# Optimization experiments

Measured on AMD Instinct MI355X. Metric: run time of the kernel, lower is better.

Reference implementation:

```python
import jax, jax.numpy as jnp
import numpy as np

NUM_NODES = 50000
NUM_EDGES = 400000
NUM_GRAPHS = 16


def _glorot(key, shape):
    fan_in, fan_out = shape[0], shape[1]
    lim = jnp.sqrt(6.0 / (fan_in + fan_out))
    return jax.random.uniform(key, shape, jnp.float32, -lim, lim)


def setup_inputs() -> dict:
    key = jax.random.key(0)
    ks = jax.random.split(key, 12)
    x = jax.random.normal(ks[0], (NUM_NODES, 3), jnp.float32)
    edge_index = jax.random.randint(ks[1], (2, NUM_EDGES), 0, NUM_NODES, jnp.int64)
    batch = jax.random.randint(ks[2], (NUM_NODES,), 0, NUM_GRAPHS, jnp.int64)
    return {
        "x": x,
        "edge_index": edge_index,
        "batch": batch,
        "W1": _glorot(ks[3], (3, 512)),   "b1": jnp.zeros((512,), jnp.float32),
        "W2": _glorot(ks[4], (512, 1024)), "b2": jnp.zeros((1024,), jnp.float32),
        "W3": _glorot(ks[5], (1024, 512)), "b3": jnp.zeros((512,), jnp.float32),
        "fcw1": _glorot(ks[6], (512, 128)), "fcb1": jnp.zeros((128,), jnp.float32),
        "fcw2": _glorot(ks[7], (128, 1)),   "fcb2": jnp.zeros((1,), jnp.float32),
    }


def _gcn_conv(x, W, b, row, col, n):
    # PyG GCNConv: h = x W; out_i = sum_{j->i} d_j^{-1/2} d_i^{-1/2} h_j + b
    # (row, col) already include self-loops; edge weights are 1.
    h = x @ W  # [N, out]
    deg = jnp.zeros((n,), h.dtype).at[col].add(1.0)  # in-degree incl. self-loop
    dis = jax.lax.rsqrt(deg)  # deg >= 1 thanks to self-loops
    norm = dis[row] * dis[col]  # [E]
    msgs = h[row] * norm[:, None]  # [E, out] gather
    return jax.ops.segment_sum(msgs, col, num_segments=n) + b


def reference(x, edge_index, batch, W1, b1, W2, b2, W3, b3, fcw1, fcb1, fcw2, fcb2):
    n = x.shape[0]
    loop = jnp.arange(n, dtype=edge_index.dtype)
    row = jnp.concatenate([edge_index[0], loop])  # source
    col = jnp.concatenate([edge_index[1], loop])  # target

    h = jax.nn.relu(_gcn_conv(x, W1, b1, row, col, n))
    h = jax.nn.relu(_gcn_conv(h, W2, b2, row, col, n))
    h = jax.nn.relu(_gcn_conv(h, W3, b3, row, col, n))

    # global mean pool over graphs in the batch
    sums = jax.ops.segment_sum(h, batch, num_segments=NUM_GRAPHS)  # [G, 512]
    cnts = jax.ops.segment_sum(jnp.ones((n,), h.dtype), batch, num_segments=NUM_GRAPHS)
    pooled = sums / jnp.maximum(cnts, 1.0)[:, None]

    out = jax.nn.relu(pooled @ fcw1 + fcb1)
    out = out @ fcw2 + fcb2  # [G, 1]
    return out
```

## Files before the change

### kernel.cpp

```cpp
#include <hip/hip_runtime.h>
#include <hip/hip_bf16.h>

#define NNODES 50000
#define NEDGES 400000
#define NGRAPH 16

typedef __attribute__((ext_vector_type(4))) float floatx4;
typedef __attribute__((ext_vector_type(8))) short short8;

typedef __attribute__((address_space(3))) unsigned int lds_uint;
typedef __attribute__((address_space(1))) const unsigned int gbl_uint;

__device__ __forceinline__ void load16_to_lds(const void* g, void* l) {
    __builtin_amdgcn_global_load_lds((gbl_uint*)g, (lds_uint*)l, 16, 0, 0);
}

__global__ __launch_bounds__(64) void zero_out_k(float* out, int n) {
    int i = blockIdx.x * 64 + threadIdx.x;
    if (i < n) out[i] = 0.0f;
}

__global__ __launch_bounds__(256) void init_k(int* deg_cnt, int* cursor,
                                              float* gsum, int* gcnt,
                                              const float* __restrict__ x,
                                              float4* __restrict__ xp, int n) {
    int i = blockIdx.x * 256 + threadIdx.x;
    if (i < n) {
        deg_cnt[i] = 0; cursor[i] = 0;
        xp[i] = make_float4(x[i * 3 + 0], x[i * 3 + 1], x[i * 3 + 2], 0.0f);
    }
    if (i < NGRAPH * 512) gsum[i] = 0.0f;
    if (i < NGRAPH) gcnt[i] = 0;
}

__global__ __launch_bounds__(256) void deg_k(const int* __restrict__ col,
                                             int* __restrict__ deg_cnt, int e) {
    int i = blockIdx.x * 256 + threadIdx.x;
    if (i < e) atomicAdd(&deg_cnt[col[i]], 1);
}

__global__ __launch_bounds__(256) void segsum_k(const int* __restrict__ cnt,
                                                int* __restrict__ segsum, int n) {
    __shared__ int sb[256];
    int seg = blockIdx.x;
    int base = seg * 1024;
    int t = threadIdx.x;
    int s = 0;
#pragma unroll
    for (int j = 0; j < 4; ++j) {
        int idx = base + t + j * 256;
        if (idx < n) s += cnt[idx];
    }
    sb[t] = s;
    __syncthreads();
    for (int off = 128; off > 0; off >>= 1) {
        if (t < off) sb[t] += sb[t + off];
        __syncthreads();
    }
    if (t == 0) segsum[seg] = sb[0];
}

__global__ __launch_bounds__(64) void segscan_k(const int* __restrict__ segsum,
                                                int* __restrict__ segbase,
                                                int* __restrict__ offs,
                                                int nseg, int n) {
    if (threadIdx.x == 0) {
        int run = 0;
        for (int s = 0; s < nseg; ++s) { segbase[s] = run; run += segsum[s]; }
        offs[n] = run;
    }
}

__global__ __launch_bounds__(1024) void offs_k(const int* __restrict__ cnt,
                                               const int* __restrict__ segbase,
                                               int* __restrict__ offs,
                                               float* __restrict__ dis, int n) {
    __shared__ int sb[1024];
    int seg = blockIdx.x;
    int t = threadIdx.x;
    int i = seg * 1024 + t;
    int c = (i < n) ? cnt[i] : 0;
    sb[t] = c;
    __syncthreads();
    for (int off = 1; off < 1024; off <<= 1) {
        int v = (t >= off) ? sb[t - off] : 0;
        __syncthreads();
        sb[t] += v;
        __syncthreads();
    }
    if (i < n) {
        offs[i] = segbase[seg] + sb[t] - c;
        dis[i]  = rsqrtf((float)(c + 1));
    }
}

__global__ __launch_bounds__(256) void scatter_k(const int* __restrict__ row,
                                                 const int* __restrict__ col,
                                                 const int* __restrict__ offs,
                                                 int* __restrict__ cursor,
                                                 int* __restrict__ ssrc,
                                                 float* __restrict__ sw,
                                                 const float* __restrict__ dis, int e) {
    int i = blockIdx.x * 256 + threadIdx.x;
    if (i >= e) return;
    int d = col[i];
    int p = offs[d] + atomicAdd(&cursor[d], 1);
    int s = row[i];
    ssrc[p] = s;
    sw[p]   = dis[s];
}

__global__ __launch_bounds__(256) void agg3_k(const float4* __restrict__ xp,
                                              float* __restrict__ out,
                                              const int* __restrict__ offs,
                                              const int* __restrict__ ssrc,
                                              const float* __restrict__ sw,
                                              const float* __restrict__ dis, int n) {
    int d = blockIdx.x * 256 + threadIdx.x;
    if (d >= n) return;
    float dd = dis[d];
    float4 xd = xp[d];
    float a0 = dd * xd.x, a1 = dd * xd.y, a2 = dd * xd.z;
    int beg = offs[d], end = offs[d + 1];
    for (int e = beg; e < end; ++e) {
        int s = ssrc[e];
        float w = sw[e];
        float4 q = xp[s];
        a0 += w * q.x; a1 += w * q.y; a2 += w * q.z;
    }
    out[d * 3 + 0] = dd * a0;
    out[d * 3 + 1] = dd * a1;
    out[d * 3 + 2] = dd * a2;
}

__global__ __launch_bounds__(256) void gemm1_k(const float* __restrict__ aggx,
                                               const float* __restrict__ W1,
                                               const float* __restrict__ b1,
                                               __hip_bfloat16* __restrict__ h1, int n) {
    int wave = threadIdx.x >> 6;
    int lane = threadIdx.x & 63;
    int d = blockIdx.x * 4 + wave;
    if (d >= n) return;
    float a0 = aggx[d * 3 + 0], a1 = aggx[d * 3 + 1], a2 = aggx[d * 3 + 2];
    int f0 = lane * 8;
    short8 ov;
#pragma unroll
    for (int j = 0; j < 8; ++j) {
        int f = f0 + j;
        float v = b1[f] + a0 * W1[f] + a1 * W1[512 + f] + a2 * W1[1024 + f];
        __hip_bfloat16 h = __float2bfloat16(fmaxf(v, 0.0f));
        ov[j] = *(short*)&h;
    }
    *(short8*)&h1[(size_t)d * 512 + f0] = ov;
}

__device__ inline float bs2f(short v) {
    return __uint_as_float(((unsigned int)(unsigned short)v) << 16);
}

__global__ __launch_bounds__(256) void agg512w_k(const __hip_bfloat16* __restrict__ in,
                                                 __hip_bfloat16* __restrict__ out,
                                                 const int* __restrict__ offs,
                                                 const int* __restrict__ ssrc,
                                                 const float* __restrict__ sw,
                                                 const float* __restrict__ dis,
                                                 const float* __restrict__ bias,
                                                 int relu, int n) {
    int wave = threadIdx.x >> 6;
    int lane = threadIdx.x & 63;
    int d = blockIdx.x * 4 + wave;
    if (d >= n) return;
    float dd = dis[d];
    short8 p = *(const short8*)&in[(size_t)d * 512 + lane * 8];
    float acc[8];
#pragma unroll
    for (int j = 0; j < 8; ++j) acc[j] = dd * bs2f(p[j]);

    int beg = offs[d], end = offs[d + 1];
    int e = beg;
    for (; e + 3 < end; e += 4) {
        int s0 = ssrc[e],     s1 = ssrc[e + 1];
        int s2 = ssrc[e + 2], s3 = ssrc[e + 3];
        float w0 = sw[e],     w1 = sw[e + 1];
        float w2 = sw[e + 2], w3 = sw[e + 3];
        short8 q0 = *(const short8*)&in[(size_t)s0 * 512 + lane * 8];
        short8 q1 = *(const short8*)&in[(size_t)s1 * 512 + lane * 8];
        short8 q2 = *(const short8*)&in[(size_t)s2 * 512 + lane * 8];
        short8 q3 = *(const short8*)&in[(size_t)s3 * 512 + lane * 8];
#pragma unroll
        for (int j = 0; j < 8; ++j) acc[j] += w0 * bs2f(q0[j]);
#pragma unroll
        for (int j = 0; j < 8; ++j) acc[j] += w1 * bs2f(q1[j]);
#pragma unroll
        for (int j = 0; j < 8; ++j) acc[j] += w2 * bs2f(q2[j]);
#pragma unroll
        for (int j = 0; j < 8; ++j) acc[j] += w3 * bs2f(q3[j]);
    }
    for (; e < end; ++e) {
        int s0 = ssrc[e];
        float w0 = sw[e];
        short8 q0 = *(const short8*)&in[(size_t)s0 * 512 + lane * 8];
#pragma unroll
        for (int j = 0; j < 8; ++j) acc[j] += w0 * bs2f(q0[j]);
    }

    short8 ov;
#pragma unroll
    for (int j = 0; j < 8; ++j) {
        float v = acc[j] * dd;
        if (bias) v += bias[lane * 8 + j];
        if (relu) v = fmaxf(v, 0.0f);
        __hip_bfloat16 h = __float2bfloat16(v);
        ov[j] = *(short*)&h;
    }
    *(short8*)&out[(size_t)d * 512 + lane * 8] = ov;
}

__global__ __launch_bounds__(256) void tcvt_k(const float* __restrict__ W2,
                                              __hip_bfloat16* __restrict__ w2t,
                                              const float* __restrict__ W3,
                                              __hip_bfloat16* __restrict__ w3t) {
    __shared__ float tile[32][33];
    int t = threadIdx.x;
    const float* W; __hip_bfloat16* Wt;
    int K, N, idx;
    if (blockIdx.x < 512) { W = W2; Wt = w2t; K = 512;  N = 1024; idx = blockIdx.x; }
    else                  { W = W3; Wt = w3t; K = 1024; N = 512;  idx = blockIdx.x - 512; }
    int nbn = N / 32;
    int bn = (idx % nbn) * 32;
    int bk = (idx / nbn) * 32;
    int c = t & 31, r0 = t >> 5;
#pragma unroll
    for (int j = 0; j < 4; ++j) {
        int r = r0 + j * 8;
        tile[r][c] = W[(size_t)(bk + r) * N + bn + c];
    }
    __syncthreads();
#pragma unroll
    for (int j = 0; j < 4; ++j) {
        int r = r0 + j * 8;
        Wt[(size_t)(bn + r) * K + bk + c] = __float2bfloat16(tile[c][r]);
    }
}

__global__ __launch_bounds__(512, 2) void mfma_gemm256_k(
        const __hip_bfloat16* __restrict__ A,
        const __hip_bfloat16* __restrict__ Bt,
        const float* __restrict__ bias,
        __hip_bfloat16* __restrict__ C,
        int M, int N, int K, int relu, int lnt) {
    __shared__ short smem[65536];

    int tid  = threadIdx.x;
    int lane = tid & 63;
    int wave = tid >> 6;
    int wm = wave >> 2;
    int wn = wave & 3;
    int fr = lane & 15;
    int kg = lane >> 4;
    int f7 = fr & 7;

    int nwg = gridDim.x;
    int wg  = (blockIdx.x & 7) * (nwg >> 3) + (blockIdx.x >> 3);
    int mt  = wg >> lnt;
    int nt  = wg & ((1 << lnt) - 1);
    int bm  = mt << 8;
    int bn  = nt << 8;

    int rsub = lane >> 3;
    int slog = (lane & 7) ^ rsub;
    const __hip_bfloat16* ga[4];
    const __hip_bfloat16* gb[4];
#pragma unroll
    for (int j = 0; j < 4; ++j) {
        int rloc = (wave * 4 + j) * 8 + rsub;
        ga[j] = A  + (size_t)(bm + rloc) * K + slog * 8;
        gb[j] = Bt + (size_t)(bn + rloc) * K + slog * 8;
    }
    int dstA = wave * 2048;

    int aoff = (wm * 128 + fr) * 64 + ((kg ^ f7) * 8);
    int boff = 16384 + (wn * 64 + fr) * 64 + ((kg ^ f7) * 8);

    floatx4 acc[8][4] = {};

    auto stage = [&](int p) {
        short* sp = &smem[p * 32768];
#pragma unroll
        for (int j = 0; j < 4; ++j) {
            load16_to_lds(ga[j], sp + dstA + j * 512);
            load16_to_lds(gb[j], sp + 16384 + dstA + j * 512);
            ga[j] += 64;
            gb[j] += 64;
        }
    };

    stage(0);
    int KT = K >> 6;
    for (int t = 0; t < KT; ++t) {
        int p = t & 1;
        __builtin_amdgcn_s_barrier();
        if (t + 1 < KT) {
            stage(p ^ 1);
            asm volatile("s_waitcnt vmcnt(8)" ::: "memory");
        } else {
            asm volatile("s_waitcnt vmcnt(0)" ::: "memory");
        }
        __builtin_amdgcn_s_barrier();

        const short* sm = &smem[p * 32768];
#pragma unroll
        for (int ks = 0; ks < 2; ++ks) {
            int kx = ks * 32;
            short8 bfr[4];
#pragma unroll
            for (int ni = 0; ni < 4; ++ni)
                bfr[ni] = *(const short8*)&sm[(boff + ni * 1024) ^ kx];
#pragma unroll
            for (int mh = 0; mh < 2; ++mh) {
                short8 afr[4];
#pragma unroll
                for (int mi = 0; mi < 4; ++mi)
                    afr[mi] = *(const short8*)&sm[(aoff + (mh * 4 + mi) * 1024) ^ kx];
                __builtin_amdgcn_s_setprio(1);
#pragma unroll
                for (int mi = 0; mi < 4; ++mi)
#pragma unroll
                    for (int ni = 0; ni < 4; ++ni)
                        acc[mh * 4 + mi][ni] = __builtin_amdgcn_mfma_f32_16x16x32_bf16(
                            afr[mi], bfr[ni], acc[mh * 4 + mi][ni], 0, 0, 0);
                __builtin_amdgcn_s_setprio(0);
            }
        }
    }

    short* Cs = smem;
    int l4 = lane >> 4;
#pragma unroll
    for (int h = 0; h < 2; ++h) {
        __builtin_amdgcn_s_barrier();
        if (wm == h) {
#pragma unroll
            for (int mi = 0; mi < 8; ++mi) {
#pragma unroll
                for (int ni = 0; ni < 4; ++ni) {
                    int rr = mi * 16 + l4 * 4;
                    int cc = wn * 64 + ni * 16 + fr;
                    float bv = bias ? bias[bn + cc] : 0.0f;
#pragma unroll
                    for (int r = 0; r < 4; ++r) {
                        float v = acc[mi][ni][r] + bv;
                        if (relu) v = fmaxf(v, 0.0f);
                        __hip_bfloat16 hh = __float2bfloat16(v);
                        Cs[(rr + r) * 264 + cc] = *(short*)&hh;
                    }
                }
            }
        }
        __builtin_amdgcn_s_barrier();
#pragma unroll
        for (int i = 0; i < 8; ++i) {
            int idx = tid + 512 * i;
            int rr = idx >> 5, cc = idx & 31;
            int grow = bm + h * 128 + rr;
            if (grow < M)
                *(short8*)&C[(size_t)grow * N + bn + cc * 8] =
                    *(const short8*)&Cs[rr * 264 + cc * 8];
        }
    }
}

__global__ __launch_bounds__(256) void pool_k(const __hip_bfloat16* __restrict__ h,
                                              const int* __restrict__ batch,
                                              float* __restrict__ gsum,
                                              int* __restrict__ gcnt, int n) {
    __shared__ float ls[NGRAPH * 512];
    __shared__ int lcnt[NGRAPH];
    int t = threadIdx.x;
    for (int i = t; i < NGRAPH * 512; i += 256) ls[i] = 0.0f;
    if (t < NGRAPH) lcnt[t] = 0;
    __syncthreads();
    for (int d = blockIdx.x; d < n; d += gridDim.x) {
        int g = batch[d];
        if (t == 0) atomicAdd(&lcnt[g], 1);
        unsigned int q = *(const unsigned int*)&h[(size_t)d * 512 + 2 * t];
        ls[g * 512 + 2 * t]     += __uint_as_float((q & 0xffffu) << 16);
        ls[g * 512 + 2 * t + 1] += __uint_as_float((q >> 16) << 16);
    }
    __syncthreads();
    for (int i = t; i < NGRAPH * 512; i += 256) atomicAdd(&gsum[i], ls[i]);
    if (t < NGRAPH) atomicAdd(&gcnt[t], lcnt[t]);
}

__global__ __launch_bounds__(128) void fc_k(const float* __restrict__ gsum,
                                            const int* __restrict__ gcnt,
                                            const float* __restrict__ fcw1,
                                            const float* __restrict__ fcb1,
                                            const float* __restrict__ fcw2,
                                            const float* __restrict__ fcb2,
                                            float* __restrict__ out) {
    int g = blockIdx.x;
    int t = threadIdx.x;
    __shared__ float pooled[512];
    __shared__ float red[128];
    float inv = 1.0f / fmaxf((float)gcnt[g], 1.0f);
    for (int i = t; i < 512; i += 128) pooled[i] = gsum[g * 512 + i] * inv;
    __syncthreads();
    float s = fcb1[t];
    for (int k = 0; k < 512; ++k) s += pooled[k] * fcw1[k * 128 + t];
    s = fmaxf(s, 0.0f);
    red[t] = s * fcw2[t];
    __syncthreads();
    for (int off = 64; off > 0; off >>= 1) {
        if (t < off) red[t] += red[t + off];
        __syncthreads();
    }
    if (t == 0) out[g] = red[0] + fcb2[0];
}

extern "C" void kernel_launch(void* const* d_in, const int* in_sizes, int n_in,
                              void* d_out, int out_size, void* d_ws, size_t ws_size,
                              hipStream_t stream) {
    const float* x    = (const float*)d_in[0];
    const int*   ei   = (const int*)d_in[1];
    const int*   batch= (const int*)d_in[2];
    const float* W1   = (const float*)d_in[3];
    const float* b1   = (const float*)d_in[4];
    const float* W2   = (const float*)d_in[5];
    const float* b2   = (const float*)d_in[6];
    const float* W3   = (const float*)d_in[7];
    const float* b3   = (const float*)d_in[8];
    const float* fcw1 = (const float*)d_in[9];
    const float* fcb1 = (const float*)d_in[10];
    const float* fcw2 = (const float*)d_in[11];
    const float* fcb2 = (const float*)d_in[12];
    float* out = (float*)d_out;

    const int N = in_sizes[0] / 3;
    const int E = in_sizes[1] / 2;
    const int Mpad = (N + 255) & ~255;
    const int nseg = (N + 1023) / 1024;
    const int* row = ei;
    const int* col = ei + E;

    size_t used = 0;
    auto need = [&](size_t bytes) {
        size_t off = used;
        used += (bytes + 255) & ~(size_t)255;
        return off;
    };
    size_t o_deg  = need((size_t)N * 4);
    size_t o_cur  = need((size_t)N * 4);
    size_t o_dis  = need((size_t)N * 4);
    size_t o_offs = need((size_t)(N + 1) * 4);
    size_t o_seg  = need((size_t)nseg * 4);
    size_t o_segb = need((size_t)nseg * 4);
    size_t o_ssrc = need((size_t)E * 4);
    size_t o_sw   = need((size_t)E * 4);
    size_t o_xp   = need((size_t)N * 16);
    size_t o_aggx = need((size_t)N * 3 * 4);
    size_t o_gsum = need((size_t)NGRAPH * 512 * 4);
    size_t o_gcnt = need((size_t)NGRAPH * 4);
    size_t o_w2t  = need((size_t)512 * 1024 * 2);
    size_t o_w3t  = need((size_t)1024 * 512 * 2);
    size_t o_bufX = need((size_t)Mpad * 512 * 2);
    size_t o_bufY = need((size_t)Mpad * 512 * 2);
    size_t o_bufZ = need((size_t)Mpad * 1024 * 2);

    if (used > ws_size) {
        hipLaunchKernelGGL(zero_out_k, dim3((out_size + 63) / 64), dim3(64), 0, stream,
                           out, out_size);
        return;
    }

    char* base = (char*)d_ws;
    int*    deg_cnt = (int*)   (base + o_deg);
    int*    cursor  = (int*)   (base + o_cur);
    float*  dis     = (float*) (base + o_dis);
    int*    offs    = (int*)   (base + o_offs);
    int*    segsum  = (int*)   (base + o_seg);
    int*    segbase = (int*)   (base + o_segb);
    int*    ssrc    = (int*)   (base + o_ssrc);
    float*  sw      = (float*) (base + o_sw);
    float4* xp      = (float4*)(base + o_xp);
    float*  aggx    = (float*) (base + o_aggx);
    float*  gsum    = (float*) (base + o_gsum);
    int*    gcnt    = (int*)   (base + o_gcnt);
    __hip_bfloat16* w2t  = (__hip_bfloat16*)(base + o_w2t);
    __hip_bfloat16* w3t  = (__hip_bfloat16*)(base + o_w3t);
    __hip_bfloat16* bufX = (__hip_bfloat16*)(base + o_bufX);
    __hip_bfloat16* bufY = (__hip_bfloat16*)(base + o_bufY);
    __hip_bfloat16* bufZ = (__hip_bfloat16*)(base + o_bufZ);
    (void)n_in;

    int gN = (N + 255) / 256;
    int gE = (E + 255) / 256;
    int gW = (N + 3) / 4;
    int nrt = Mpad / 256;

    hipLaunchKernelGGL(init_k, dim3(gN), dim3(256), 0, stream, deg_cnt, cursor, gsum, gcnt, x, xp, N);
    hipLaunchKernelGGL(deg_k, dim3(gE), dim3(256), 0, stream, col, deg_cnt, E);
    hipLaunchKernelGGL(segsum_k, dim3(nseg), dim3(256), 0, stream, deg_cnt, segsum, N);
    hipLaunchKernelGGL(segscan_k, dim3(1), dim3(64), 0, stream, segsum, segbase, offs, nseg, N);
    hipLaunchKernelGGL(offs_k, dim3(nseg), dim3(1024), 0, stream, deg_cnt, segbase, offs, dis, N);
    hipLaunchKernelGGL(scatter_k, dim3(gE), dim3(256), 0, stream, row, col, offs, cursor, ssrc, sw, dis, E);

    hipLaunchKernelGGL(tcvt_k, dim3(1024), dim3(256), 0, stream, W2, w2t, W3, w3t);

    hipLaunchKernelGGL(agg3_k, dim3(gN), dim3(256), 0, stream, xp, aggx, offs, ssrc, sw, dis, N);
    hipLaunchKernelGGL(gemm1_k, dim3(gW), dim3(256), 0, stream, aggx, W1, b1, bufX, N);

    hipLaunchKernelGGL(agg512w_k, dim3(gW), dim3(256), 0, stream, bufX, bufY, offs, ssrc, sw, dis,
                       (const float*)nullptr, 0, N);
    hipLaunchKernelGGL(mfma_gemm256_k, dim3(nrt * 4), dim3(512), 0, stream,
                       bufY, w2t, b2, bufZ, N, 1024, 512, 1, 2);

    hipLaunchKernelGGL(mfma_gemm256_k, dim3(nrt * 2), dim3(512), 0, stream,
                       bufZ, w3t, (const float*)nullptr, bufX, N, 512, 1024, 0, 1);
    hipLaunchKernelGGL(agg512w_k, dim3(gW), dim3(256), 0, stream, bufX, bufY, offs, ssrc, sw, dis,
                       b3, 1, N);

    hipLaunchKernelGGL(pool_k, dim3(256), dim3(256), 0, stream, bufY, batch, gsum, gcnt, N);
    hipLaunchKernelGGL(fc_k, dim3(NGRAPH), dim3(128), 0, stream, gsum, gcnt, fcw1, fcb1, fcw2, fcb2, out);
}
```

Baseline: 592.5 us.

## Switch GEMM to 4-stage K=32 pipeline with fragment-ordered LDS layout

The bf16 MFMA GEMM now stages K in chunks of 32 instead of 64 and keeps four LDS buffers in flight instead of two. Each global-to-LDS load writes a 16-row by 32-k subtile laid out so every lane can read its MFMA fragment contiguously, which removes the XOR swizzle. The intent is to hide global latency behind a deeper prefetch and simplify LDS addressing. The trade-off is twice as many barriers per K, and the unswizzled layout may cause LDS bank conflicts on the direct-to-LDS writes or the fragment reads.

```diff
diff --git a/kernel.cpp b/kernel.cpp
--- a/kernel.cpp
+++ b/kernel.cpp
@@ -257,8 +257,6 @@
     int wm = wave >> 2;
     int wn = wave & 3;
     int fr = lane & 15;
-    int kg = lane >> 4;
-    int f7 = fr & 7;
 
     int nwg = gridDim.x;
     int wg  = (blockIdx.x & 7) * (nwg >> 3) + (blockIdx.x >> 3);
@@ -267,72 +265,71 @@
     int bm  = mt << 8;
     int bn  = nt << 8;
 
-    int rsub = lane >> 3;
-    int slog = (lane & 7) ^ rsub;
-    const __hip_bfloat16* ga[4];
-    const __hip_bfloat16* gb[4];
-#pragma unroll
-    for (int j = 0; j < 4; ++j) {
-        int rloc = (wave * 4 + j) * 8 + rsub;
-        ga[j] = A  + (size_t)(bm + rloc) * K + slog * 8;
-        gb[j] = Bt + (size_t)(bn + rloc) * K + slog * 8;
-    }
-    int dstA = wave * 2048;
-
-    int aoff = (wm * 128 + fr) * 64 + ((kg ^ f7) * 8);
-    int boff = 16384 + (wn * 64 + fr) * 64 + ((kg ^ f7) * 8);
+    int r = lane & 15;
+    int s = lane >> 4;
+    const __hip_bfloat16* ga[2];
+    const __hip_bfloat16* gb[2];
+#pragma unroll
+    for (int j = 0; j < 2; ++j) {
+        int gsub = 2 * wave + j;
+        ga[j] = A  + (size_t)(bm + gsub * 16 + r) * K + s * 8;
+        gb[j] = Bt + (size_t)(bn + gsub * 16 + r) * K + s * 8;
+    }
 
     floatx4 acc[8][4] = {};
 
     auto stage = [&](int p) {
-        short* sp = &smem[p * 32768];
-#pragma unroll
-        for (int j = 0; j < 4; ++j) {
-            load16_to_lds(ga[j], sp + dstA + j * 512);
-            load16_to_lds(gb[j], sp + 16384 + dstA + j * 512);
-            ga[j] += 64;
-            gb[j] += 64;
+        short* sp = &smem[p * 16384];
+#pragma unroll
+        for (int j = 0; j < 2; ++j) {
+            load16_to_lds(ga[j], sp + (2 * wave + j) * 512);
+            load16_to_lds(gb[j], sp + 8192 + (2 * wave + j) * 512);
+            ga[j] += 32;
+            gb[j] += 32;
         }
     };
 
-    stage(0);
-    int KT = K >> 6;
-    for (int t = 0; t < KT; ++t) {
-        int p = t & 1;
+    auto compute = [&](int p) {
+        const short* sm = &smem[p * 16384];
+        short8 bfr[4];
+#pragma unroll
+        for (int ni = 0; ni < 4; ++ni)
+            bfr[ni] = *(const short8*)&sm[8192 + (wn * 4 + ni) * 512 + lane * 8];
+#pragma unroll
+        for (int mh = 0; mh < 2; ++mh) {
+            short8 afr[4];
+#pragma unroll
+            for (int mi = 0; mi < 4; ++mi)
+                afr[mi] = *(const short8*)&sm[(wm * 8 + mh * 4 + mi) * 512 + lane * 8];
+            __builtin_amdgcn_s_setprio(1);
+#pragma unroll
+            for (int mi = 0; mi < 4; ++mi)
+#pragma unroll
+                for (int ni = 0; ni < 4; ++ni)
+                    acc[mh * 4 + mi][ni] = __builtin_amdgcn_mfma_f32_16x16x32_bf16(
+                        afr[mi], bfr[ni], acc[mh * 4 + mi][ni], 0, 0, 0);
+            __builtin_amdgcn_s_setprio(0);
+        }
+    };
+
+    int KT = K >> 5;
+    stage(0); stage(1); stage(2);
+    for (int t = 0; t < KT - 3; ++t) {
+        stage((t + 3) & 3);
+        asm volatile("s_waitcnt vmcnt(12)" ::: "memory");
         __builtin_amdgcn_s_barrier();
-        if (t + 1 < KT) {
-            stage(p ^ 1);
-            asm volatile("s_waitcnt vmcnt(8)" ::: "memory");
-        } else {
-            asm volatile("s_waitcnt vmcnt(0)" ::: "memory");
-        }
+        compute(t & 3);
         __builtin_amdgcn_s_barrier();
-
-        const short* sm = &smem[p * 32768];
-#pragma unroll
-        for (int ks = 0; ks < 2; ++ks) {
-            int kx = ks * 32;
-            short8 bfr[4];
-#pragma unroll
-            for (int ni = 0; ni < 4; ++ni)
-                bfr[ni] = *(const short8*)&sm[(boff + ni * 1024) ^ kx];
-#pragma unroll
-            for (int mh = 0; mh < 2; ++mh) {
-                short8 afr[4];
-#pragma unroll
-                for (int mi = 0; mi < 4; ++mi)
-                    afr[mi] = *(const short8*)&sm[(aoff + (mh * 4 + mi) * 1024) ^ kx];
-                __builtin_amdgcn_s_setprio(1);
-#pragma unroll
-                for (int mi = 0; mi < 4; ++mi)
-#pragma unroll
-                    for (int ni = 0; ni < 4; ++ni)
-                        acc[mh * 4 + mi][ni] = __builtin_amdgcn_mfma_f32_16x16x32_bf16(
-                            afr[mi], bfr[ni], acc[mh * 4 + mi][ni], 0, 0, 0);
-                __builtin_amdgcn_s_setprio(0);
-            }
-        }
-    }
+    }
+    asm volatile("s_waitcnt vmcnt(8)" ::: "memory");
+    __builtin_amdgcn_s_barrier();
+    compute((KT - 3) & 3);
+    asm volatile("s_waitcnt vmcnt(4)" ::: "memory");
+    __builtin_amdgcn_s_barrier();
+    compute((KT - 2) & 3);
+    asm volatile("s_waitcnt vmcnt(0)" ::: "memory");
+    __builtin_amdgcn_s_barrier();
+    compute((KT - 1) & 3);
 
     short* Cs = smem;
     int l4 = lane >> 4;
@@ -348,11 +345,11 @@
                     int cc = wn * 64 + ni * 16 + fr;
                     float bv = bias ? bias[bn + cc] : 0.0f;
 #pragma unroll
-                    for (int r = 0; r < 4; ++r) {
-                        float v = acc[mi][ni][r] + bv;
+                    for (int q = 0; q < 4; ++q) {
+                        float v = acc[mi][ni][q] + bv;
                         if (relu) v = fmaxf(v, 0.0f);
                         __hip_bfloat16 hh = __float2bfloat16(v);
-                        Cs[(rr + r) * 264 + cc] = *(short*)&hh;
+                        Cs[(rr + q) * 264 + cc] = *(short*)&hh;
                     }
                 }
             }
@@ -406,10 +403,10 @@
     float inv = 1.0f / fmaxf((float)gcnt[g], 1.0f);
     for (int i = t; i < 512; i += 128) pooled[i] = gsum[g * 512 + i] * inv;
     __syncthreads();
-    float s = fcb1[t];
-    for (int k = 0; k < 512; ++k) s += pooled[k] * fcw1[k * 128 + t];
-    s = fmaxf(s, 0.0f);
-    red[t] = s * fcw2[t];
+    float sacc = fcb1[t];
+    for (int k = 0; k < 512; ++k) sacc += pooled[k] * fcw1[k * 128 + t];
+    sacc = fmaxf(sacc, 0.0f);
+    red[t] = sacc * fcw2[t];
     __syncthreads();
     for (int off = 64; off > 0; off >>= 1) {
         if (t < off) red[t] += red[t + off];
```

New measurement: 612.2 us. 3.3% more time.

## Fuse final GCN aggregation with global mean pooling via per-graph node permutation

Applied to the files above, without the earlier changes.

Builds a per-graph node permutation (count, prefix, place kernels) so the last aggregation can run grouped by graph. Bias, ReLU and pooling are applied in registers and reduced in LDS, then atomically added into the per-graph sums. This removes the write and re-read of the final 512-wide activation buffer and the separate pool kernel. It adds three small setup kernels and a memset, and the per-graph split may balance load unevenly across blocks. It also inserts an explicit LDS waitcnt before a barrier in the GEMM.

```diff
diff --git a/kernel.cpp b/kernel.cpp
--- a/kernel.cpp
+++ b/kernel.cpp
@@ -4,6 +4,7 @@
 #define NNODES 50000
 #define NEDGES 400000
 #define NGRAPH 16
+#define NBG 64
 
 typedef __attribute__((ext_vector_type(4))) float floatx4;
 typedef __attribute__((ext_vector_type(8))) short short8;
@@ -21,16 +22,23 @@
 }
 
 __global__ __launch_bounds__(256) void init_k(int* deg_cnt, int* cursor,
-                                              float* gsum, int* gcnt,
+                                              float* gsum, int* gdeg,
                                               const float* __restrict__ x,
-                                              float4* __restrict__ xp, int n) {
-    int i = blockIdx.x * 256 + threadIdx.x;
+                                              float4* __restrict__ xp,
+                                              const int* __restrict__ batch, int n) {
+    __shared__ int h[NGRAPH];
+    int t = threadIdx.x;
+    if (t < NGRAPH) h[t] = 0;
+    __syncthreads();
+    int i = blockIdx.x * 256 + t;
     if (i < n) {
         deg_cnt[i] = 0; cursor[i] = 0;
         xp[i] = make_float4(x[i * 3 + 0], x[i * 3 + 1], x[i * 3 + 2], 0.0f);
+        atomicAdd(&h[batch[i]], 1);
     }
     if (i < NGRAPH * 512) gsum[i] = 0.0f;
-    if (i < NGRAPH) gcnt[i] = 0;
+    __syncthreads();
+    if (t < NGRAPH && h[t]) atomicAdd(&gdeg[t], h[t]);
 }
 
 __global__ __launch_bounds__(256) void deg_k(const int* __restrict__ col,
@@ -108,6 +116,35 @@
     int s = row[i];
     ssrc[p] = s;
     sw[p]   = dis[s];
+}
+
+__global__ __launch_bounds__(64) void gpfx_k(const int* __restrict__ gdeg,
+                                             int* __restrict__ goffs) {
+    if (threadIdx.x == 0) {
+        int run = 0;
+        for (int g = 0; g < NGRAPH; ++g) { goffs[g] = run; run += gdeg[g]; }
+    }
+}
+
+__global__ __launch_bounds__(256) void gplace_k(const int* __restrict__ batch,
+                                                const int* __restrict__ goffs,
+                                                int* __restrict__ gcur,
+                                                int* __restrict__ perm, int n) {
+    __shared__ int h[NGRAPH];
+    __shared__ int basev[NGRAPH];
+    int t = threadIdx.x;
+    if (t < NGRAPH) h[t] = 0;
+    __syncthreads();
+    int i = blockIdx.x * 256 + t;
+    int g = 0, r = 0;
+    if (i < n) {
+        g = batch[i];
+        r = atomicAdd(&h[g], 1);
+    }
+    __syncthreads();
+    if (t < NGRAPH) basev[t] = h[t] ? atomicAdd(&gcur[t], h[t]) : 0;
+    __syncthreads();
+    if (i < n) perm[goffs[g] + basev[g] + r] = i;
 }
 
 __global__ __launch_bounds__(256) void agg3_k(const float4* __restrict__ xp,
@@ -163,9 +200,7 @@
                                                  const int* __restrict__ offs,
                                                  const int* __restrict__ ssrc,
                                                  const float* __restrict__ sw,
-                                                 const float* __restrict__ dis,
-                                                 const float* __restrict__ bias,
-                                                 int relu, int n) {
+                                                 const float* __restrict__ dis, int n) {
     int wave = threadIdx.x >> 6;
     int lane = threadIdx.x & 63;
     int d = blockIdx.x * 4 + wave;
@@ -207,13 +242,94 @@
     short8 ov;
 #pragma unroll
     for (int j = 0; j < 8; ++j) {
-        float v = acc[j] * dd;
-        if (bias) v += bias[lane * 8 + j];
-        if (relu) v = fmaxf(v, 0.0f);
-        __hip_bfloat16 h = __float2bfloat16(v);
+        __hip_bfloat16 h = __float2bfloat16(acc[j] * dd);
         ov[j] = *(short*)&h;
     }
     *(short8*)&out[(size_t)d * 512 + lane * 8] = ov;
+}
+
+__global__ __launch_bounds__(256) void aggpool_k(const __hip_bfloat16* __restrict__ in,
+                                                 const int* __restrict__ perm,
+                                                 const int* __restrict__ goffs,
+                                                 const int* __restrict__ gdeg,
+                                                 const int* __restrict__ offs,
+                                                 const int* __restrict__ ssrc,
+                                                 const float* __restrict__ sw,
+                                                 const float* __restrict__ dis,
+                                                 const float* __restrict__ bias,
+                                                 float* __restrict__ gsum) {
+    __shared__ float lsw[4 * 512];
+    int t = threadIdx.x;
+    int wave = t >> 6;
+    int lane = t & 63;
+    int g = blockIdx.x & (NGRAPH - 1);
+    int s = blockIdx.x >> 4;
+    for (int i = t; i < 4 * 512; i += 256) lsw[i] = 0.0f;
+    int cnt = gdeg[g];
+    int per = (cnt + NBG - 1) / NBG;
+    int beg = s * per;
+    int end = min(cnt, beg + per);
+    int gb  = goffs[g];
+    float bj[8];
+#pragma unroll
+    for (int j = 0; j < 8; ++j) bj[j] = bias[lane * 8 + j];
+    __syncthreads();
+
+    for (int ii = beg + wave; ii < end; ii += 4) {
+        int d = perm[gb + ii];
+        float dd = dis[d];
+        short8 p = *(const short8*)&in[(size_t)d * 512 + lane * 8];
+        float acc[8];
+#pragma unroll
+        for (int j = 0; j < 8; ++j) acc[j] = dd * bs2f(p[j]);
+
+        int eb = offs[d], ee = offs[d + 1];
+        int e = eb;
+        for (; e + 3 < ee; e += 4) {
+            int s0 = ssrc[e],     s1 = ssrc[e + 1];
+            int s2 = ssrc[e + 2], s3 = ssrc[e + 3];
+            float w0 = sw[e],     w1 = sw[e + 1];
+            float w2 = sw[e + 2], w3 = sw[e + 3];
+            short8 q0 = *(const short8*)&in[(size_t)s0 * 512 + lane * 8];
+            short8 q1 = *(const short8*)&in[(size_t)s1 * 512 + lane * 8];
+            short8 q2 = *(const short8*)&in[(size_t)s2 * 512 + lane * 8];
+            short8 q3 = *(const short8*)&in[(size_t)s3 * 512 + lane * 8];
+#pragma unroll
+            for (int j = 0; j < 8; ++j) acc[j] += w0 * bs2f(q0[j]);
+#pragma unroll
+            for (int j = 0; j < 8; ++j) acc[j] += w1 * bs2f(q1[j]);
+#pragma unroll
+            for (int j = 0; j < 8; ++j) acc[j] += w2 * bs2f(q2[j]);
+#pragma unroll
+            for (int j = 0; j < 8; ++j) acc[j] += w3 * bs2f(q3[j]);
+        }
+        for (; e < ee; ++e) {
+            int s0 = ssrc[e];
+            float w0 = sw[e];
+            short8 q0 = *(const short8*)&in[(size_t)s0 * 512 + lane * 8];
+#pragma unroll
+            for (int j = 0; j < 8; ++j) acc[j] += w0 * bs2f(q0[j]);
+        }
+
+        float* mb = &lsw[wave * 512 + lane * 8];
+        float4 a0 = *(float4*)mb;
+        float4 a1 = *((float4*)mb + 1);
+        a0.x += fmaxf(acc[0] * dd + bj[0], 0.0f);
+        a0.y += fmaxf(acc[1] * dd + bj[1], 0.0f);
+        a0.z += fmaxf(acc[2] * dd + bj[2], 0.0f);
+        a0.w += fmaxf(acc[3] * dd + bj[3], 0.0f);
+        a1.x += fmaxf(acc[4] * dd + bj[4], 0.0f);
+        a1.y += fmaxf(acc[5] * dd + bj[5], 0.0f);
+        a1.z += fmaxf(acc[6] * dd + bj[6], 0.0f);
+        a1.w += fmaxf(acc[7] * dd + bj[7], 0.0f);
+        *(float4*)mb = a0;
+        *((float4*)mb + 1) = a1;
+    }
+    __syncthreads();
+    for (int f = t; f < 512; f += 256) {
+        float v = lsw[f] + lsw[512 + f] + lsw[1024 + f] + lsw[1536 + f];
+        atomicAdd(&gsum[g * 512 + f], v);
+    }
 }
 
 __global__ __launch_bounds__(256) void tcvt_k(const float* __restrict__ W2,
@@ -357,6 +473,7 @@
                 }
             }
         }
+        asm volatile("s_waitcnt lgkmcnt(0)" ::: "memory");
         __builtin_amdgcn_s_barrier();
 #pragma unroll
         for (int i = 0; i < 8; ++i) {
@@ -370,30 +487,8 @@
     }
 }
 
-__global__ __launch_bounds__(256) void pool_k(const __hip_bfloat16* __restrict__ h,
-                                              const int* __restrict__ batch,
-                                              float* __restrict__ gsum,
-                                              int* __restrict__ gcnt, int n) {
-    __shared__ float ls[NGRAPH * 512];
-    __shared__ int lcnt[NGRAPH];
-    int t = threadIdx.x;
-    for (int i = t; i < NGRAPH * 512; i += 256) ls[i] = 0.0f;
-    if (t < NGRAPH) lcnt[t] = 0;
-    __syncthreads();
-    for (int d = blockIdx.x; d < n; d += gridDim.x) {
-        int g = batch[d];
-        if (t == 0) atomicAdd(&lcnt[g], 1);
-        unsigned int q = *(const unsigned int*)&h[(size_t)d * 512 + 2 * t];
-        ls[g * 512 + 2 * t]     += __uint_as_float((q & 0xffffu) << 16);
-        ls[g * 512 + 2 * t + 1] += __uint_as_float((q >> 16) << 16);
-    }
-    __syncthreads();
-    for (int i = t; i < NGRAPH * 512; i += 256) atomicAdd(&gsum[i], ls[i]);
-    if (t < NGRAPH) atomicAdd(&gcnt[t], lcnt[t]);
-}
-
 __global__ __launch_bounds__(128) void fc_k(const float* __restrict__ gsum,
-                                            const int* __restrict__ gcnt,
+                                            const int* __restrict__ gdeg,
                                             const float* __restrict__ fcw1,
                                             const float* __restrict__ fcb1,
                                             const float* __restrict__ fcw2,
@@ -403,13 +498,13 @@
     int t = threadIdx.x;
     __shared__ float pooled[512];
     __shared__ float red[128];
-    float inv = 1.0f / fmaxf((float)gcnt[g], 1.0f);
+    float inv = 1.0f / fmaxf((float)gdeg[g], 1.0f);
     for (int i = t; i < 512; i += 128) pooled[i] = gsum[g * 512 + i] * inv;
     __syncthreads();
-    float s = fcb1[t];
-    for (int k = 0; k < 512; ++k) s += pooled[k] * fcw1[k * 128 + t];
-    s = fmaxf(s, 0.0f);
-    red[t] = s * fcw2[t];
+    float sacc = fcb1[t];
+    for (int k = 0; k < 512; ++k) sacc += pooled[k] * fcw1[k * 128 + t];
+    sacc = fmaxf(sacc, 0.0f);
+    red[t] = sacc * fcw2[t];
     __syncthreads();
     for (int off = 64; off > 0; off >>= 1) {
         if (t < off) red[t] += red[t + off];
@@ -460,7 +555,10 @@
     size_t o_xp   = need((size_t)N * 16);
     size_t o_aggx = need((size_t)N * 3 * 4);
     size_t o_gsum = need((size_t)NGRAPH * 512 * 4);
-    size_t o_gcnt = need((size_t)NGRAPH * 4);
+    size_t o_gdeg = need((size_t)NGRAPH * 4);
+    size_t o_gcur = need((size_t)NGRAPH * 4);
+    size_t o_goff = need((size_t)(NGRAPH + 1) * 4);
+    size_t o_perm = need((size_t)N * 4);
     size_t o_w2t  = need((size_t)512 * 1024 * 2);
     size_t o_w3t  = need((size_t)1024 * 512 * 2);
     size_t o_bufX = need((size_t)Mpad * 512 * 2);
@@ -485,7 +583,10 @@
     float4* xp      = (float4*)(base + o_xp);
     float*  aggx    = (float*) (base + o_aggx);
     float*  gsum    = (float*) (base + o_gsum);
-    int*    gcnt    = (int*)   (base + o_gcnt);
+    int*    gdeg    = (int*)   (base + o_gdeg);
+    int*    gcur    = (int*)   (base + o_gcur);
+    int*    goffs   = (int*)   (base + o_goff);
+    int*    perm    = (int*)   (base + o_perm);
     __hip_bfloat16* w2t  = (__hip_bfloat16*)(base + o_w2t);
     __hip_bfloat16* w3t  = (__hip_bfloat16*)(base + o_w3t);
     __hip_bfloat16* bufX = (__hip_bfloat16*)(base + o_bufX);
@@ -498,28 +599,31 @@
     int gW = (N + 3) / 4;
     int nrt = Mpad / 256;
 
-    hipLaunchKernelGGL(init_k, dim3(gN), dim3(256), 0, stream, deg_cnt, cursor, gsum, gcnt, x, xp, N);
+    hipMemsetAsync(base + o_gdeg, 0, 512, stream);
+
+    hipLaunchKernelGGL(init_k, dim3(gN), dim3(256), 0, stream, deg_cnt, cursor, gsum, gdeg, x, xp, batch, N);
     hipLaunchKernelGGL(deg_k, dim3(gE), dim3(256), 0, stream, col, deg_cnt, E);
     hipLaunchKernelGGL(segsum_k, dim3(nseg), dim3(256), 0, stream, deg_cnt, segsum, N);
     hipLaunchKernelGGL(segscan_k, dim3(1), dim3(64), 0, stream, segsum, segbase, offs, nseg, N);
     hipLaunchKernelGGL(offs_k, dim3(nseg), dim3(1024), 0, stream, deg_cnt, segbase, offs, dis, N);
     hipLaunchKernelGGL(scatter_k, dim3(gE), dim3(256), 0, stream, row, col, offs, cursor, ssrc, sw, dis, E);
 
+    hipLaunchKernelGGL(gpfx_k, dim3(1), dim3(64), 0, stream, gdeg, goffs);
+    hipLaunchKernelGGL(gplace_k, dim3(gN), dim3(256), 0, stream, batch, goffs, gcur, perm, N);
+
     hipLaunchKernelGGL(tcvt_k, dim3(1024), dim3(256), 0, stream, W2, w2t, W3, w3t);
 
     hipLaunchKernelGGL(agg3_k, dim3(gN), dim3(256), 0, stream, xp, aggx, offs, ssrc, sw, dis, N);
     hipLaunchKernelGGL(gemm1_k, dim3(gW), dim3(256), 0, stream, aggx, W1, b1, bufX, N);
 
-    hipLaunchKernelGGL(agg512w_k, dim3(gW), dim3(256), 0, stream, bufX, bufY, offs, ssrc, sw, dis,
-                       (const float*)nullptr, 0, N);
+    hipLaunchKernelGGL(agg512w_k, dim3(gW), dim3(256), 0, stream, bufX, bufY, offs, ssrc, sw, dis, N);
     hipLaunchKernelGGL(mfma_gemm256_k, dim3(nrt * 4), dim3(512), 0, stream,
                        bufY, w2t, b2, bufZ, N, 1024, 512, 1, 2);
 
     hipLaunchKernelGGL(mfma_gemm256_k, dim3(nrt * 2), dim3(512), 0, stream,
                        bufZ, w3t, (const float*)nullptr, bufX, N, 512, 1024, 0, 1);
-    hipLaunchKernelGGL(agg512w_k, dim3(gW), dim3(256), 0, stream, bufX, bufY, offs, ssrc, sw, dis,
-                       b3, 1, N);
-
-    hipLaunchKernelGGL(pool_k, dim3(256), dim3(256), 0, stream, bufY, batch, gsum, gcnt, N);
-    hipLaunchKernelGGL(fc_k, dim3(NGRAPH), dim3(128), 0, stream, gsum, gcnt, fcw1, fcb1, fcw2, fcb2, out);
-}
+    hipLaunchKernelGGL(aggpool_k, dim3(NGRAPH * NBG), dim3(256), 0, stream,
+                       bufX, perm, goffs, gdeg, offs, ssrc, sw, dis, b3, gsum);
+
+    hipLaunchKernelGGL(fc_k, dim3(NGRAPH), dim3(128), 0, stream, gsum, gdeg, fcw1, fcb1, fcw2, fcb2, out);
+}
```

After: 502.1 us. 1.18x faster.
